# Kernel optimization log

Measured on AMD Instinct MI355X. Metric: run time of the kernel, lower is better.

The kernel has to match this reference:

```python
import jax, jax.numpy as jnp
import numpy as np

B, N, DH, DE = 256, 64, 256, 64
OUT, ND, RO, TGT = 256, 11, 512, 12
DIN = DH + DE  # duvenaud message size = |h| + |e|


def setup_inputs() -> dict:
    key = jax.random.key(0)
    ks = jax.random.split(key, 16)
    s = 0.05
    # binary adjacency with mean degree ~5 so degrees fall in d = 0..10
    g = (jax.random.uniform(ks[0], (B, N, N)) < 0.08).astype(jnp.float32)
    h_in = jax.random.normal(ks[1], (B, N, DH), jnp.float32)
    e = jax.random.normal(ks[2], (B, N, N, DE), jnp.float32)
    # per-degree update matrices (layer0 in = DH+DE, layer1 in = OUT+DE = 320 too)
    Wu0 = jax.random.normal(ks[3], (ND, DIN, OUT), jnp.float32) * s
    Wu1 = jax.random.normal(ks[4], (ND, OUT + DE, OUT), jnp.float32) * s
    # readout projections, one per layer (h_in, h1, h2 all have dim 256)
    R = jax.random.normal(ks[5], (3, DH, RO), jnp.float32) * s
    # NNet MLP: RO -> 128 -> 256 -> 128 -> TGT
    fc0_w = jax.random.normal(ks[6], (RO, 128), jnp.float32) * s
    fc0_b = jnp.zeros((128,), jnp.float32)
    fc1_w = jax.random.normal(ks[7], (128, 256), jnp.float32) * s
    fc1_b = jnp.zeros((256,), jnp.float32)
    fc2_w = jax.random.normal(ks[8], (256, 128), jnp.float32) * s
    fc2_b = jnp.zeros((128,), jnp.float32)
    fc3_w = jax.random.normal(ks[9], (128, TGT), jnp.float32) * s
    fc3_b = jnp.zeros((TGT,), jnp.float32)
    return dict(g=g, h_in=h_in, e=e, Wu0=Wu0, Wu1=Wu1, R=R,
                fc0_w=fc0_w, fc0_b=fc0_b, fc1_w=fc1_w, fc1_b=fc1_b,
                fc2_w=fc2_w, fc2_b=fc2_b, fc3_w=fc3_w, fc3_b=fc3_b)


def _forward(g, h_in, e, Wu0, Wu1, R, fcs):
    deg = jnp.sum(g, axis=2)  # [B,N]
    # one-hot over supported degrees 0..ND-1; unsupported degree -> all-zero row -> zero update
    onehot = (deg[..., None] == jnp.arange(ND, dtype=g.dtype)).astype(g.dtype)  # [B,N,ND]
    hs = [h_in]
    h = h_in
    for W in (Wu0, Wu1):
        m_h = jnp.einsum('bvw,bwd->bvd', g, h)   # sum of neighbor states
        m_e = jnp.einsum('bvw,bvwe->bve', g, e)  # sum of incident edge features
        m = jnp.concatenate([m_h, m_e], axis=-1)  # [B,N,320]
        per_deg = jax.nn.sigmoid(jnp.einsum('bvi,dio->bvdo', m, W))  # [B,N,ND,OUT]
        h = jnp.einsum('bvdo,bvd->bvo', per_deg, onehot)  # degree-grouped select
        hs.append(h)
    # readout: per-layer projection, masked softmax per node, sum over nodes+layers
    acc = jnp.zeros((h_in.shape[0], R.shape[-1]), h_in.dtype)
    for l, hl in enumerate(hs):
        z = jnp.einsum('bvd,do->bvo', hl, R[l])  # [B,N,RO]
        mask = jnp.any(z != 0, axis=-1, keepdims=True).astype(z.dtype)  # mask all-zero rows
        acc = acc + jnp.sum(jax.nn.softmax(z, axis=-1) * mask, axis=1)
    x = acc
    for w, b in fcs[:-1]:
        x = jax.nn.relu(x @ w + b)
    w, b = fcs[-1]
    return x @ w + b


def reference(g, h_in, e, Wu0, Wu1, R, fc0_w, fc0_b, fc1_w, fc1_b, fc2_w, fc2_b, fc3_w, fc3_b):
    fcs = [(fc0_w, fc0_b), (fc1_w, fc1_b), (fc2_w, fc2_b), (fc3_w, fc3_b)]
    return _forward(g, h_in, e, Wu0, Wu1, R, fcs)
```

## Files before the change

kernel.cpp:

```cpp
#include <hip/hip_runtime.h>
#include <hip/hip_bf16.h>

#define BB 256
#define NN 64
#define NNODES 16384
#define ND 11
#define TGT 12
#define NTILE (NNODES / 64 + ND)

#define NB_DEG   64
#define NB_MEDEG 4096
#define NB_CVTR  96
#define NB_CVTW  352
#define NB_LIGHT (NB_DEG + NB_MEDEG + NB_CVTR + NB_CVTW)

typedef __attribute__((ext_vector_type(8))) short s16x8;
typedef __attribute__((ext_vector_type(4))) float f32x4;

__device__ __forceinline__ float sig1(float v) { return 1.f / (1.f + __expf(-v)); }
__device__ __forceinline__ float bf2f(unsigned short u) {
    union { unsigned int i; float f; } v; v.i = ((unsigned int)u) << 16; return v.f;
}
__device__ __forceinline__ unsigned short f2bf(float f) {
    __hip_bfloat16 b = __float2bfloat16(f);
    return *reinterpret_cast<unsigned short*>(&b);
}

__global__ __launch_bounds__(256) void k_prep_light(
        const float* __restrict__ g, const float* __restrict__ e,
        const float* __restrict__ R,
        const float* __restrict__ Wu0, const float* __restrict__ Wu1,
        unsigned short* __restrict__ Mb,
        unsigned short* __restrict__ Rtf, unsigned short* __restrict__ Wtf0,
        unsigned short* __restrict__ Wtf1, int* __restrict__ degidx,
        int* __restrict__ rowmap, int* __restrict__ cnt,
        unsigned short* __restrict__ hb1, unsigned short* __restrict__ hb2) {
    __shared__ int hist[ND];
    __shared__ int baseg[ND];
    int bid = blockIdx.x;
    const int tid = threadIdx.x;
    const int lane = tid & 63, wv = tid >> 6;
    const int gq = lane >> 4, c16 = lane & 15;

    if (bid < NB_DEG) {
        if (tid < ND) hist[tid] = 0;
        __syncthreads();
        const int node = bid * 256 + tid;
        const float4* gr = reinterpret_cast<const float4*>(g + (size_t)node * 64);
        float s = 0.f;
        #pragma unroll
        for (int j = 0; j < 16; ++j) { float4 v = gr[j]; s += v.x + v.y + v.z + v.w; }
        const int di = (int)(s + 0.5f);
        const bool valid = di < ND;
        int pl = 0;
        if (valid) pl = atomicAdd(&hist[di], 1);
        __syncthreads();
        if (tid < ND) baseg[tid] = hist[tid] ? atomicAdd(&cnt[tid], hist[tid]) : 0;
        __syncthreads();
        degidx[node] = valid ? di : -1;
        if (valid) {
            rowmap[di * NNODES + baseg[di] + pl] = node;
        } else {
            uint4 z = make_uint4(0, 0, 0, 0);
            uint4* p1 = reinterpret_cast<uint4*>(hb1 + (size_t)node * 256);
            uint4* p2 = reinterpret_cast<uint4*>(hb2 + (size_t)node * 256);
            #pragma unroll
            for (int k = 0; k < 32; ++k) { p1[k] = z; p2[k] = z; }
        }
        return;
    }
    bid -= NB_DEG;

    if (bid < NB_MEDEG) {
        const int node = bid * 4 + wv;
        const float gv = g[(size_t)node * 64 + lane];
        unsigned long long mask = __ballot(gv != 0.f);
        if (__popcll(mask) > 10) return;
        const float* eb = e + (size_t)node * 4096;
        float acc = 0.f;
        while (mask) {
            int w = __builtin_ctzll(mask); mask &= mask - 1;
            acc += eb[w * 64 + lane];
        }
        Mb[(size_t)node * 320 + 256 + lane] = f2bf(acc);
        return;
    }
    bid -= NB_MEDEG;

    if (bid < NB_CVTR) {
        const int l = bid >> 5, cb = bid & 31;
        const float* Rl = R + (size_t)l * 256 * 512;
        unsigned short* outB = Rtf + ((size_t)l * 32 + cb) * 8 * 512;
        const int col = cb * 16 + c16;
        #pragma unroll
        for (int it = 0; it < 2; ++it) {
            int ks = wv + it * 4;
            unsigned short tmp[8];
            #pragma unroll
            for (int j = 0; j < 8; ++j)
                tmp[j] = f2bf(Rl[(size_t)(ks * 32 + gq * 8 + j) * 512 + col]);
            *reinterpret_cast<uint4*>(&outB[(size_t)ks * 512 + lane * 8]) =
                *reinterpret_cast<const uint4*>(tmp);
        }
        return;
    }
    bid -= NB_CVTR;

    {
        const int wsel = bid / 176, rem = bid % 176;
        const int d = rem >> 4, cb = rem & 15;
        const float* Wd = (wsel ? Wu1 : Wu0) + (size_t)d * 320 * 256;
        unsigned short* outB = (wsel ? Wtf1 : Wtf0) + ((size_t)d * 16 + cb) * 10 * 512;
        const int col = cb * 16 + c16;
        #pragma unroll
        for (int it = 0; it < 3; ++it) {
            int ks = wv + it * 4;
            if (ks < 10) {
                unsigned short tmp[8];
                #pragma unroll
                for (int j = 0; j < 8; ++j)
                    tmp[j] = f2bf(Wd[(size_t)(ks * 32 + gq * 8 + j) * 256 + col]);
                *reinterpret_cast<uint4*>(&outB[(size_t)ks * 512 + lane * 8]) =
                    *reinterpret_cast<const uint4*>(tmp);
            }
        }
    }
}

__global__ __launch_bounds__(256) void k_prep_mh(
        const float* __restrict__ g, const float* __restrict__ h_in,
        unsigned short* __restrict__ Mb, unsigned short* __restrict__ hb0) {
    __shared__ __align__(16) unsigned short hs[NN * 256];
    const int b = blockIdx.x;
    const int tid = threadIdx.x;
    const int lane = tid & 63, wv = tid >> 6;
    const float4* hin4 = reinterpret_cast<const float4*>(h_in) + (size_t)b * 4096;
    ushort4* hb0b = reinterpret_cast<ushort4*>(hb0 + (size_t)b * NN * 256);
    #pragma unroll
    for (int j = 0; j < 16; ++j) {
        int i = j * 256 + tid;
        float4 v = hin4[i];
        ushort4 u = make_ushort4(f2bf(v.x), f2bf(v.y), f2bf(v.z), f2bf(v.w));
        *reinterpret_cast<ushort4*>(&hs[i * 4]) = u;
        hb0b[i] = u;
    }
    __syncthreads();
    for (int s = 0; s < 16; ++s) {
        const int v = wv * 16 + s;
        float gval = g[((size_t)b * 64 + v) * 64 + lane];
        unsigned long long mask = __ballot(gval != 0.f);
        if (__popcll(mask) > 10) continue;
        float4 acc = make_float4(0.f, 0.f, 0.f, 0.f);
        while (mask) {
            int w = __builtin_ctzll(mask); mask &= mask - 1;
            ushort4 hv = *reinterpret_cast<const ushort4*>(&hs[w * 256 + lane * 4]);
            acc.x += bf2f(hv.x); acc.y += bf2f(hv.y);
            acc.z += bf2f(hv.z); acc.w += bf2f(hv.w);
        }
        ushort4 u = make_ushort4(f2bf(acc.x), f2bf(acc.y), f2bf(acc.z), f2bf(acc.w));
        *reinterpret_cast<ushort4*>(&Mb[((size_t)b * 64 + v) * 320 + lane * 4]) = u;
    }
}

__global__ __launch_bounds__(256) void k_update(
        const unsigned short* __restrict__ Mb,
        const unsigned short* __restrict__ Wtf,
        const int* __restrict__ rowmap,
        const int* __restrict__ cnt,
        unsigned short* __restrict__ hout) {
    __shared__ __align__(16) unsigned short AsCt[64 * 320];
    __shared__ int nmap[64];
    __shared__ int scnt[ND];
    const int tid = threadIdx.x;
    if (tid < ND) scnt[tid] = cnt[tid];
    __syncthreads();
    const int half = blockIdx.x & 1;
    int rem = blockIdx.x >> 1, d = 0;
    for (; d < ND; ++d) { int td = (scnt[d] + 63) >> 6; if (rem < td) break; rem -= td; }
    if (d >= ND) return;
    const int cd = scnt[d];
    const int base = rem * 64;
    if (tid < 64) {
        int s = base + tid;
        nmap[tid] = (s < cd) ? rowmap[d * NNODES + s] : -1;
    }
    __syncthreads();
    const int grow = tid >> 2, gseg = tid & 3;
    {
        int node = nmap[grow];
        if (node < 0) node = rowmap[d * NNODES];
        const char* src = reinterpret_cast<const char*>(Mb + (size_t)node * 320);
        char* dstA = reinterpret_cast<char*>(AsCt) + grow * 640;
        #pragma unroll
        for (int j = 0; j < 10; ++j) {
            int c = gseg + 4 * j;
            uint4 v = *reinterpret_cast<const uint4*>(src + c * 16);
            *reinterpret_cast<uint4*>(dstA + ((c ^ (grow & 7)) * 16)) = v;
        }
    }
    __syncthreads();
    const int w = tid >> 6, lane = tid & 63, gq = lane >> 4, c16 = lane & 15;
    const int swz = (c16 & 7) << 4;
    const int cb0 = half * 8 + w * 2;
    f32x4 acc[4][2];
    #pragma unroll
    for (int rt = 0; rt < 4; ++rt) {
        acc[rt][0] = (f32x4){0.f, 0.f, 0.f, 0.f};
        acc[rt][1] = (f32x4){0.f, 0.f, 0.f, 0.f};
    }
    #pragma unroll
    for (int ks = 0; ks < 10; ++ks) {
        s16x8 af[4], bf[2];
        #pragma unroll
        for (int rt = 0; rt < 4; ++rt)
            af[rt] = *reinterpret_cast<const s16x8*>(
                reinterpret_cast<const char*>(AsCt) + (rt * 16 + c16) * 640 +
                ((ks * 64 + gq * 16) ^ swz));
        #pragma unroll
        for (int ct = 0; ct < 2; ++ct)
            bf[ct] = *reinterpret_cast<const s16x8*>(
                &Wtf[((((size_t)d * 16 + cb0 + ct) * 10 + ks) * 64 + lane) * 8]);
        #pragma unroll
        for (int rt = 0; rt < 4; ++rt) {
            acc[rt][0] = __builtin_amdgcn_mfma_f32_16x16x32_bf16(af[rt], bf[0], acc[rt][0], 0, 0, 0);
            acc[rt][1] = __builtin_amdgcn_mfma_f32_16x16x32_bf16(af[rt], bf[1], acc[rt][1], 0, 0, 0);
        }
    }
    __syncthreads();
    #pragma unroll
    for (int rt = 0; rt < 4; ++rt)
        #pragma unroll
        for (int jj = 0; jj < 4; ++jj) {
            int row = rt * 16 + gq * 4 + jj;
            AsCt[row * 128 + w * 32 + c16]      = f2bf(sig1(acc[rt][0][jj]));
            AsCt[row * 128 + w * 32 + 16 + c16] = f2bf(sig1(acc[rt][1][jj]));
        }
    __syncthreads();
    {
        const int node = nmap[grow];
        if (node >= 0) {
            const uint4* srcC = reinterpret_cast<const uint4*>(&AsCt[grow * 128]);
            uint4* dst = reinterpret_cast<uint4*>(hout + (size_t)node * 256 + half * 128);
            #pragma unroll
            for (int j = 0; j < 4; ++j) dst[gseg * 4 + j] = srcC[gseg * 4 + j];
        }
    }
}

__global__ __launch_bounds__(256) void k_mh_sparse(const float* __restrict__ g,
                                                   const unsigned short* __restrict__ hb,
                                                   unsigned short* __restrict__ Mb) {
    __shared__ __align__(16) unsigned short hs[NN * 256];
    const int b = blockIdx.x;
    const int tid = threadIdx.x;
    {
        const uint4* src = reinterpret_cast<const uint4*>(hb) + (size_t)b * 2048;
        uint4* dst = reinterpret_cast<uint4*>(hs);
        #pragma unroll
        for (int j = 0; j < 8; ++j) dst[j * 256 + tid] = src[j * 256 + tid];
    }
    __syncthreads();
    const int wv = tid >> 6, lane = tid & 63;
    for (int s = 0; s < 16; ++s) {
        const int v = wv * 16 + s;
        float gval = g[((size_t)b * 64 + v) * 64 + lane];
        unsigned long long mask = __ballot(gval != 0.f);
        if (__popcll(mask) > 10) continue;
        float4 acc = make_float4(0.f, 0.f, 0.f, 0.f);
        while (mask) {
            int w = __builtin_ctzll(mask); mask &= mask - 1;
            ushort4 hv = *reinterpret_cast<const ushort4*>(&hs[w * 256 + lane * 4]);
            acc.x += bf2f(hv.x); acc.y += bf2f(hv.y);
            acc.z += bf2f(hv.z); acc.w += bf2f(hv.w);
        }
        ushort4 u = make_ushort4(f2bf(acc.x), f2bf(acc.y), f2bf(acc.z), f2bf(acc.w));
        *reinterpret_cast<ushort4*>(&Mb[((size_t)b * 64 + v) * 320 + lane * 4]) = u;
    }
}

__global__ __launch_bounds__(256) void k_readout_mlp(
        const unsigned short* __restrict__ hb0,
        const unsigned short* __restrict__ hb1,
        const unsigned short* __restrict__ hb2,
        const unsigned short* __restrict__ Rtf,
        const int* __restrict__ degidx,
        const float* __restrict__ fc0w, const float* __restrict__ fc0b,
        const float* __restrict__ fc1w, const float* __restrict__ fc1b,
        const float* __restrict__ fc2w, const float* __restrict__ fc2b,
        const float* __restrict__ fc3w, const float* __restrict__ fc3b,
        float* __restrict__ out) {
    const int b = blockIdx.x;
    const int tid = threadIdx.x;
    const int w = tid >> 6, lane = tid & 63, gq = lane >> 4, c16 = lane & 15;
    __shared__ __align__(16) unsigned short Ah[64 * 256];
    __shared__ float x0[512];
    __shared__ float red2[4][64];
    __shared__ __align__(16) float red3[64];
    __shared__ float flags[64];
    __shared__ float part[256];
    __shared__ float x1[128], x2[256], x3[128];
    if (tid < 64) flags[tid] = (degidx[b * 64 + tid] >= 0) ? 1.f : 0.f;
    x0[tid] = 0.f; x0[tid + 256] = 0.f;
    const int swz = (c16 & 7) << 4;

    for (int layer = 0; layer < 3; ++layer) {
        const unsigned short* hb = (layer == 0) ? hb0 : ((layer == 1) ? hb1 : hb2);
        {
            const char* src = reinterpret_cast<const char*>(hb + (size_t)b * 64 * 256);
            #pragma unroll
            for (int j = 0; j < 8; ++j) {
                int l = j * 4096 + tid * 16;
                int row = l >> 9;
                int wb = l & 511;
                uint4 v = *reinterpret_cast<const uint4*>(src + l);
                *reinterpret_cast<uint4*>(
                    reinterpret_cast<char*>(Ah) + row * 512 + (wb ^ ((row & 7) << 4))) = v;
            }
        }
        __syncthreads();
        f32x4 acc[4][8];
        #pragma unroll
        for (int rt = 0; rt < 4; ++rt)
            #pragma unroll
            for (int ct = 0; ct < 8; ++ct) acc[rt][ct] = (f32x4){0.f, 0.f, 0.f, 0.f};
        #pragma unroll
        for (int ks = 0; ks < 8; ++ks) {
            s16x8 af[4], bf[8];
            #pragma unroll
            for (int rt = 0; rt < 4; ++rt)
                af[rt] = *reinterpret_cast<const s16x8*>(
                    reinterpret_cast<const char*>(Ah) + (rt * 16 + c16) * 512 +
                    ((ks * 64 + gq * 16) ^ swz));
            #pragma unroll
            for (int ct = 0; ct < 8; ++ct)
                bf[ct] = *reinterpret_cast<const s16x8*>(
                    &Rtf[((((size_t)layer * 32 + w * 8 + ct) * 8 + ks) * 64 + lane) * 8]);
            #pragma unroll
            for (int rt = 0; rt < 4; ++rt)
                #pragma unroll
                for (int ct = 0; ct < 8; ++ct)
                    acc[rt][ct] = __builtin_amdgcn_mfma_f32_16x16x32_bf16(af[rt], bf[ct], acc[rt][ct], 0, 0, 0);
        }
        float rs[4][4];
        #pragma unroll
        for (int rt = 0; rt < 4; ++rt) {
            #pragma unroll
            for (int j = 0; j < 4; ++j) rs[rt][j] = 0.f;
            #pragma unroll
            for (int ct = 0; ct < 8; ++ct) {
                #pragma unroll
                for (int j = 0; j < 4; ++j) {
                    float p = __expf(acc[rt][ct][j]);
                    acc[rt][ct][j] = p;
                    rs[rt][j] += p;
                }
            }
        }
        #pragma unroll
        for (int rt = 0; rt < 4; ++rt)
            #pragma unroll
            for (int j = 0; j < 4; ++j) {
                float s = rs[rt][j];
                #pragma unroll
                for (int m = 1; m <= 8; m <<= 1) s += __shfl_xor(s, m);
                rs[rt][j] = s;
            }
        if (c16 == 0) {
            #pragma unroll
            for (int rt = 0; rt < 4; ++rt)
                #pragma unroll
                for (int j = 0; j < 4; ++j)
                    red2[w][rt * 16 + gq * 4 + j] = rs[rt][j];
        }
        __syncthreads();
        if (tid < 64) {
            float s = red2[0][tid] + red2[1][tid] + red2[2][tid] + red2[3][tid];
            red3[tid] = ((layer == 0) ? 1.f : flags[tid]) / s;
        }
        __syncthreads();
        f32x4 iv[4];
        #pragma unroll
        for (int rt = 0; rt < 4; ++rt)
            iv[rt] = *reinterpret_cast<const f32x4*>(&red3[rt * 16 + gq * 4]);
        #pragma unroll
        for (int ct = 0; ct < 8; ++ct) {
            f32x4 t = (f32x4){0.f, 0.f, 0.f, 0.f};
            #pragma unroll
            for (int rt = 0; rt < 4; ++rt) t += acc[rt][ct] * iv[rt];
            float v = t[0] + t[1] + t[2] + t[3];
            v += __shfl_xor(v, 16);
            v += __shfl_xor(v, 32);
            if (lane < 16) x0[w * 128 + ct * 16 + lane] += v;
        }
        __syncthreads();
    }
    {
        const int o = tid & 127, half = tid >> 7;
        float a = 0.f;
        const int i0 = half * 256;
        for (int i = 0; i < 256; ++i) a = fmaf(x0[i0 + i], fc0w[(size_t)(i0 + i) * 128 + o], a);
        part[tid] = a;
    }
    __syncthreads();
    if (tid < 128) x1[tid] = fmaxf(fc0b[tid] + part[tid] + part[tid + 128], 0.f);
    __syncthreads();
    {
        float a = fc1b[tid];
        for (int i = 0; i < 128; ++i) a = fmaf(x1[i], fc1w[(size_t)i * 256 + tid], a);
        x2[tid] = fmaxf(a, 0.f);
    }
    __syncthreads();
    {
        const int o = tid & 127, half = tid >> 7;
        float a = 0.f;
        const int i0 = half * 128;
        for (int i = 0; i < 128; ++i) a = fmaf(x2[i0 + i], fc2w[(size_t)(i0 + i) * 128 + o], a);
        part[tid] = a;
    }
    __syncthreads();
    if (tid < 128) x3[tid] = fmaxf(fc2b[tid] + part[tid] + part[tid + 128], 0.f);
    __syncthreads();
    if (tid < TGT) {
        float a = fc3b[tid];
        for (int i = 0; i < 128; ++i) a = fmaf(x3[i], fc3w[(size_t)i * TGT + tid], a);
        out[(size_t)b * TGT + tid] = a;
    }
}

extern "C" void kernel_launch(void* const* d_in, const int* in_sizes, int n_in,
                              void* d_out, int out_size, void* d_ws, size_t ws_size,
                              hipStream_t stream) {
    (void)in_sizes; (void)n_in; (void)out_size; (void)ws_size;
    const float* g    = (const float*)d_in[0];
    const float* h_in = (const float*)d_in[1];
    const float* e    = (const float*)d_in[2];
    const float* Wu0  = (const float*)d_in[3];
    const float* Wu1  = (const float*)d_in[4];
    const float* R    = (const float*)d_in[5];
    const float* fc0w = (const float*)d_in[6];
    const float* fc0b = (const float*)d_in[7];
    const float* fc1w = (const float*)d_in[8];
    const float* fc1b = (const float*)d_in[9];
    const float* fc2w = (const float*)d_in[10];
    const float* fc2b = (const float*)d_in[11];
    const float* fc3w = (const float*)d_in[12];
    const float* fc3b = (const float*)d_in[13];
    float* out = (float*)d_out;

    char* p = (char*)d_ws;
    unsigned short* Mb   = (unsigned short*)p; p += (size_t)NNODES * 320 * 2;
    unsigned short* hb0  = (unsigned short*)p; p += (size_t)NNODES * 256 * 2;
    unsigned short* hb1  = (unsigned short*)p; p += (size_t)NNODES * 256 * 2;
    unsigned short* hb2  = (unsigned short*)p; p += (size_t)NNODES * 256 * 2;
    unsigned short* Rtf  = (unsigned short*)p; p += (size_t)3 * 32 * 8 * 512 * 2;
    unsigned short* Wtf0 = (unsigned short*)p; p += (size_t)ND * 16 * 10 * 512 * 2;
    unsigned short* Wtf1 = (unsigned short*)p; p += (size_t)ND * 16 * 10 * 512 * 2;
    int* degidx = (int*)p;                     p += (size_t)NNODES * 4;
    int* rowmap = (int*)p;                     p += (size_t)ND * NNODES * 4;
    int* cnt    = (int*)p;                     p += 1024;

    hipMemsetAsync(cnt, 0, ND * sizeof(int), stream);
    k_prep_light<<<NB_LIGHT, 256, 0, stream>>>(g, e, R, Wu0, Wu1,
                                               Mb, Rtf, Wtf0, Wtf1,
                                               degidx, rowmap, cnt, hb1, hb2);
    k_prep_mh<<<BB, 256, 0, stream>>>(g, h_in, Mb, hb0);
    k_update<<<2 * NTILE, 256, 0, stream>>>(Mb, Wtf0, rowmap, cnt, hb1);
    k_mh_sparse<<<BB, 256, 0, stream>>>(g, hb1, Mb);
    k_update<<<2 * NTILE, 256, 0, stream>>>(Mb, Wtf1, rowmap, cnt, hb2);
    k_readout_mlp<<<BB, 256, 0, stream>>>(hb0, hb1, hb2, Rtf, degidx,
                                          fc0w, fc0b, fc1w, fc1b, fc2w, fc2b, fc3w, fc3b, out);
}
```

Baseline: 123.4 us.

## Fuse second-layer neighbor aggregation into the degree-grouped update kernel

```diff
diff --git a/kernel.cpp b/kernel.cpp
--- a/kernel.cpp
+++ b/kernel.cpp
@@ -162,8 +162,11 @@
     }
 }
 
+template<bool FUSE_MH>
 __global__ __launch_bounds__(256) void k_update(
         const unsigned short* __restrict__ Mb,
+        const unsigned short* __restrict__ hb_in,
+        const float* __restrict__ g,
         const unsigned short* __restrict__ Wtf,
         const int* __restrict__ rowmap,
         const int* __restrict__ cnt,
@@ -185,8 +188,38 @@
         nmap[tid] = (s < cd) ? rowmap[d * NNODES + s] : -1;
     }
     __syncthreads();
-    const int grow = tid >> 2, gseg = tid & 3;
-    {
+    const int wv = tid >> 6, lane = tid & 63;
+    if (FUSE_MH) {
+        for (int s = 0; s < 16; ++s) {
+            const int row = wv * 16 + s;
+            int node = nmap[row];
+            if (node < 0) node = rowmap[d * NNODES];
+            const float gval = g[(size_t)node * 64 + lane];
+            unsigned long long mask = __ballot(gval != 0.f);
+            const int bbase = node & ~63;
+            float4 acc = make_float4(0.f, 0.f, 0.f, 0.f);
+            while (mask) {
+                int w = __builtin_ctzll(mask); mask &= mask - 1;
+                ushort4 hv = *reinterpret_cast<const ushort4*>(
+                    &hb_in[((size_t)(bbase + w)) * 256 + lane * 4]);
+                acc.x += bf2f(hv.x); acc.y += bf2f(hv.y);
+                acc.z += bf2f(hv.z); acc.w += bf2f(hv.w);
+            }
+            ushort4 u = make_ushort4(f2bf(acc.x), f2bf(acc.y), f2bf(acc.z), f2bf(acc.w));
+            char* dstA = reinterpret_cast<char*>(AsCt) + row * 640;
+            const int cg = lane >> 1;
+            *reinterpret_cast<ushort4*>(
+                dstA + ((cg ^ (row & 7)) * 16 + (lane & 1) * 8)) = u;
+            if (lane < 16) {
+                ushort4 me = *reinterpret_cast<const ushort4*>(
+                    &Mb[(size_t)node * 320 + 256 + lane * 4]);
+                const int cm = 32 + (lane >> 1);
+                *reinterpret_cast<ushort4*>(
+                    dstA + ((cm ^ (row & 7)) * 16 + (lane & 1) * 8)) = me;
+            }
+        }
+    } else {
+        const int grow = tid >> 2, gseg = tid & 3;
         int node = nmap[grow];
         if (node < 0) node = rowmap[d * NNODES];
         const char* src = reinterpret_cast<const char*>(Mb + (size_t)node * 320);
@@ -199,9 +232,9 @@
         }
     }
     __syncthreads();
-    const int w = tid >> 6, lane = tid & 63, gq = lane >> 4, c16 = lane & 15;
+    const int gq = lane >> 4, c16 = lane & 15;
     const int swz = (c16 & 7) << 4;
-    const int cb0 = half * 8 + w * 2;
+    const int cb0 = half * 8 + wv * 2;
     f32x4 acc[4][2];
     #pragma unroll
     for (int rt = 0; rt < 4; ++rt) {
@@ -232,11 +265,12 @@
         #pragma unroll
         for (int jj = 0; jj < 4; ++jj) {
             int row = rt * 16 + gq * 4 + jj;
-            AsCt[row * 128 + w * 32 + c16]      = f2bf(sig1(acc[rt][0][jj]));
-            AsCt[row * 128 + w * 32 + 16 + c16] = f2bf(sig1(acc[rt][1][jj]));
+            AsCt[row * 128 + wv * 32 + c16]      = f2bf(sig1(acc[rt][0][jj]));
+            AsCt[row * 128 + wv * 32 + 16 + c16] = f2bf(sig1(acc[rt][1][jj]));
         }
     __syncthreads();
     {
+        const int grow = tid >> 2, gseg = tid & 3;
         const int node = nmap[grow];
         if (node >= 0) {
             const uint4* srcC = reinterpret_cast<const uint4*>(&AsCt[grow * 128]);
@@ -244,37 +278,6 @@
             #pragma unroll
             for (int j = 0; j < 4; ++j) dst[gseg * 4 + j] = srcC[gseg * 4 + j];
         }
-    }
-}
-
-__global__ __launch_bounds__(256) void k_mh_sparse(const float* __restrict__ g,
-                                                   const unsigned short* __restrict__ hb,
-                                                   unsigned short* __restrict__ Mb) {
-    __shared__ __align__(16) unsigned short hs[NN * 256];
-    const int b = blockIdx.x;
-    const int tid = threadIdx.x;
-    {
-        const uint4* src = reinterpret_cast<const uint4*>(hb) + (size_t)b * 2048;
-        uint4* dst = reinterpret_cast<uint4*>(hs);
-        #pragma unroll
-        for (int j = 0; j < 8; ++j) dst[j * 256 + tid] = src[j * 256 + tid];
-    }
-    __syncthreads();
-    const int wv = tid >> 6, lane = tid & 63;
-    for (int s = 0; s < 16; ++s) {
-        const int v = wv * 16 + s;
-        float gval = g[((size_t)b * 64 + v) * 64 + lane];
-        unsigned long long mask = __ballot(gval != 0.f);
-        if (__popcll(mask) > 10) continue;
-        float4 acc = make_float4(0.f, 0.f, 0.f, 0.f);
-        while (mask) {
-            int w = __builtin_ctzll(mask); mask &= mask - 1;
-            ushort4 hv = *reinterpret_cast<const ushort4*>(&hs[w * 256 + lane * 4]);
-            acc.x += bf2f(hv.x); acc.y += bf2f(hv.y);
-            acc.z += bf2f(hv.z); acc.w += bf2f(hv.w);
-        }
-        ushort4 u = make_ushort4(f2bf(acc.x), f2bf(acc.y), f2bf(acc.z), f2bf(acc.w));
-        *reinterpret_cast<ushort4*>(&Mb[((size_t)b * 64 + v) * 320 + lane * 4]) = u;
     }
 }
 
@@ -464,9 +467,8 @@
                                                Mb, Rtf, Wtf0, Wtf1,
                                                degidx, rowmap, cnt, hb1, hb2);
     k_prep_mh<<<BB, 256, 0, stream>>>(g, h_in, Mb, hb0);
-    k_update<<<2 * NTILE, 256, 0, stream>>>(Mb, Wtf0, rowmap, cnt, hb1);
-    k_mh_sparse<<<BB, 256, 0, stream>>>(g, hb1, Mb);
-    k_update<<<2 * NTILE, 256, 0, stream>>>(Mb, Wtf1, rowmap, cnt, hb2);
+    k_update<false><<<2 * NTILE, 256, 0, stream>>>(Mb, nullptr, g, Wtf0, rowmap, cnt, hb1);
+    k_update<true><<<2 * NTILE, 256, 0, stream>>>(Mb, hb1, g, Wtf1, rowmap, cnt, hb2);
     k_readout_mlp<<<BB, 256, 0, stream>>>(hb0, hb1, hb2, Rtf, degidx,
                                           fc0w, fc0b, fc1w, fc1b, fc2w, fc2b, fc3w, fc3b, out);
 }
```

New measurement: 159.7 us. 29.4% more time.
